# Kernel optimization log

Hardware: AMD Instinct MI355X
Metric: run time of the kernel (lower is better)

The kernel has to match this reference:

```python
import jax, jax.numpy as jnp
import numpy as np

B, S, D = 16, 2048, 512
CODEBOOK = 8192


def setup_inputs() -> dict:
    key = jax.random.key(0)
    k1, k2, k3 = jax.random.split(key, 3)
    x = jax.random.normal(k1, (B, S, D), dtype=jnp.float32)
    input_length = jax.random.randint(k2, (B,), 1, S + 1).astype(jnp.int32)
    # kaiming-uniform-ish init of the codebook
    bound = float(np.sqrt(6.0 / D))
    embed = jax.random.uniform(k3, (CODEBOOK, D), dtype=jnp.float32,
                               minval=-bound, maxval=bound)
    return {"x": x, "input_length": input_length, "embed": embed}


def reference(x, input_length, embed):
    # x: [B, S, D] float32, input_length: [B] int32, embed: [C, D] float32
    b, s, d = x.shape
    mask = jnp.arange(s)[None, :] < input_length[:, None]  # [B, S]
    x = x.astype(jnp.float32)

    # Euclidean cdist (clamped, sqrt), negated; argmax = nearest code.
    x2 = jnp.sum(x * x, axis=-1, keepdims=True)            # [B, S, 1]
    e2 = jnp.sum(embed * embed, axis=-1)                   # [C]
    xy = jnp.einsum('bsd,cd->bsc', x, embed)               # [B, S, C]
    dist = -jnp.sqrt(jnp.clip(x2 + e2[None, None, :] - 2.0 * xy, 0.0))

    embed_ind = jnp.argmax(dist, axis=-1)                  # [B, S] int
    quantize = embed[embed_ind]                            # [B, S, D]

    # pack/unpack in the torch code reduces to masking per-token results
    quantize = jnp.where(mask[..., None], quantize, 0.0)
    embed_ind = jnp.where(mask, embed_ind, -1)
    return quantize, embed_ind
```

## Files before the change

### kernel.cpp

```cpp
#include <hip/hip_runtime.h>
#include <cfloat>

typedef _Float16 half8  __attribute__((ext_vector_type(8)));
typedef short    bf16x8 __attribute__((ext_vector_type(8)));
typedef float    floatx4 __attribute__((ext_vector_type(4)));
typedef int      intx4  __attribute__((ext_vector_type(4)));
typedef unsigned long long ull;

#define NBATCH 16
#define NSEQ   2048
#define ND     512
#define NC     8192
#define NTOK   (NBATCH * NSEQ)
#define NTT    (NTOK / 128)
#define NCT    (NC / 128)
#define KQ     (ND / 64)
#define SEGY   8
#define MARGIN 0.35f

#define XSCALE 8.0f
#define ESCALE 64.0f
#define SCORE_SCALE (2.0f / (XSCALE * ESCALE))

typedef const void __attribute__((address_space(1)))* gp_t;
typedef void       __attribute__((address_space(3)))* lp_t;
__device__ __forceinline__ void cp16(lp_t l, gp_t g) {
  __builtin_amdgcn_global_load_lds(g, l, 16, 0, 0);
}

__global__ __launch_bounds__(256) void prep_embed(const float* __restrict__ embed,
                                                  char* __restrict__ qe,
                                                  float* __restrict__ se,
                                                  _Float16* __restrict__ eh,
                                                  _Float16* __restrict__ el,
                                                  float* __restrict__ e2) {
  int wave = threadIdx.x >> 6, lane = threadIdx.x & 63;
  int c = blockIdx.x * 4 + wave;
  const float* row = embed + (size_t)c * ND;
  float4 v0 = ((const float4*)row)[lane * 2];
  float4 v1 = ((const float4*)row)[lane * 2 + 1];
  float vs[8] = {v0.x, v0.y, v0.z, v0.w, v1.x, v1.y, v1.z, v1.w};
  float am = 0.f, s = 0.f;
#pragma unroll
  for (int q = 0; q < 8; ++q) { am = fmaxf(am, fabsf(vs[q])); s = fmaf(vs[q], vs[q], s); }
#pragma unroll
  for (int m = 1; m < 64; m <<= 1) {
    am = fmaxf(am, __shfl_xor(am, m, 64));
    s += __shfl_xor(s, m, 64);
  }
  float inv = am > 0.f ? 127.f / am : 0.f;
  ull pk = 0; half8 h, l;
#pragma unroll
  for (int q = 0; q < 8; ++q) {
    int qv = (int)rintf(vs[q] * inv);
    qv = min(127, max(-127, qv));
    pk |= (ull)(unsigned char)(signed char)qv << (8 * q);
    float sv = ESCALE * vs[q];
    _Float16 hh = (_Float16)sv;
    h[q] = hh;
    l[q] = (_Float16)(sv - (float)hh);
  }
  ((ull*)(qe + (size_t)c * ND))[lane] = pk;
  ((half8*)(eh + (size_t)c * ND))[lane] = h;
  ((half8*)(el + (size_t)c * ND))[lane] = l;
  if (lane == 0) { se[c] = am / 127.f; e2[c] = s; }
}

__global__ __launch_bounds__(256) void prep_xq(const float* __restrict__ x,
                                               char* __restrict__ qx,
                                               float* __restrict__ sx) {
  int wave = threadIdx.x >> 6, lane = threadIdx.x & 63;
  int t = blockIdx.x * 4 + wave;
  const float* row = x + (size_t)t * ND;
  float4 v0 = ((const float4*)row)[lane * 2];
  float4 v1 = ((const float4*)row)[lane * 2 + 1];
  float vs[8] = {v0.x, v0.y, v0.z, v0.w, v1.x, v1.y, v1.z, v1.w};
  float am = 0.f;
#pragma unroll
  for (int q = 0; q < 8; ++q) am = fmaxf(am, fabsf(vs[q]));
#pragma unroll
  for (int m = 1; m < 64; m <<= 1) am = fmaxf(am, __shfl_xor(am, m, 64));
  float inv = am > 0.f ? 127.f / am : 0.f;
  ull pk = 0;
#pragma unroll
  for (int q = 0; q < 8; ++q) {
    int qv = (int)rintf(vs[q] * inv);
    qv = min(127, max(-127, qv));
    pk |= (ull)(unsigned char)(signed char)qv << (8 * q);
  }
  ((ull*)(qx + (size_t)t * ND))[lane] = pk;
  if (lane == 0) sx[t] = am / 127.f;
}

__global__ __launch_bounds__(256) void vq_init(unsigned long long* __restrict__ pKey,
                                               int* __restrict__ cnt) {
  int i = blockIdx.x * 256 + threadIdx.x;
  pKey[i] = ~0ULL;
  if (i < NCT) cnt[i] = 0;
}

__global__ __launch_bounds__(256) void vq_approx(
    const char* __restrict__ qx, const float* __restrict__ sx,
    const int* __restrict__ len,
    const char* __restrict__ qe, const float* __restrict__ se,
    const float* __restrict__ e2g,
    float* __restrict__ tMin) {
  __shared__ char sXb[3][128 * 64];
  __shared__ char sEb[3][128 * 64];

  const int gid = blockIdx.x;
  const int tt = (gid >> 9) * 8 + (gid & 7);
  const int ct = (gid & 511) >> 3;
  const int b = tt >> 4, s0 = (tt & 15) * 128;
  if (s0 >= len[b]) return;
  const int row0 = tt * 128, code0 = ct * 128;

  const int tid = threadIdx.x, wave = tid >> 6, lane = tid & 63;
  const int quad = lane >> 4, lid = lane & 15;
  const int wr = wave >> 1, wc = wave & 1;

  const int r0 = tid >> 2;
  const int csrc = (tid & 3) ^ ((tid >> 3) & 3);
  const int ldsb0 = wave * 1024;
  const int ldsb1 = 4096 + wave * 1024;

  const int cswz = quad ^ ((lid >> 1) & 3);
  int aoff[4], boff[4];
#pragma unroll
  for (int i = 0; i < 4; ++i) aoff[i] = (wr * 64 + i * 16 + lid) * 64 + cswz * 16;
#pragma unroll
  for (int j = 0; j < 4; ++j) boff[j] = (wc * 64 + j * 16 + lid) * 64 + cswz * 16;

  const char* pxb = qx + (size_t)(row0 + r0) * ND + csrc * 16;
  const char* peb = qe + (size_t)(code0 + r0) * ND + csrc * 16;

  intx4 acc[4][4];
#pragma unroll
  for (int i = 0; i < 4; ++i)
#pragma unroll
    for (int j = 0; j < 4; ++j) acc[i][j] = (intx4){0, 0, 0, 0};

#define STAGE(bufi, kt) do { \
    cp16((lp_t)&sXb[bufi][ldsb0], (gp_t)(pxb + (kt) * 64)); \
    cp16((lp_t)&sXb[bufi][ldsb1], (gp_t)(pxb + 64 * ND + (kt) * 64)); \
    cp16((lp_t)&sEb[bufi][ldsb0], (gp_t)(peb + (kt) * 64)); \
    cp16((lp_t)&sEb[bufi][ldsb1], (gp_t)(peb + 64 * ND + (kt) * 64)); } while (0)

  STAGE(0, 0);
  STAGE(1, 1);
  asm volatile("s_waitcnt vmcnt(4)" ::: "memory");
  __builtin_amdgcn_s_barrier();

#pragma unroll
  for (int kt = 0; kt < KQ; ++kt) {
    const int buf = kt % 3;
    if (kt + 2 < KQ) STAGE((kt + 2) % 3, kt + 2);
    const char* A = sXb[buf];
    const char* B = sEb[buf];
    intx4 av[4], bv[4];
#pragma unroll
    for (int j = 0; j < 4; ++j) bv[j] = *(const intx4*)&B[boff[j]];
#pragma unroll
    for (int i = 0; i < 4; ++i) av[i] = *(const intx4*)&A[aoff[i]];
    __builtin_amdgcn_s_setprio(1);
#pragma unroll
    for (int i = 0; i < 4; ++i)
#pragma unroll
      for (int j = 0; j < 4; ++j)
        acc[i][j] = __builtin_amdgcn_mfma_i32_16x16x64_i8(av[i], bv[j], acc[i][j], 0, 0, 0);
    __builtin_amdgcn_s_setprio(0);
    if (kt < KQ - 1) {
      if (kt <= KQ - 3) { asm volatile("s_waitcnt vmcnt(4)" ::: "memory"); }
      else              { asm volatile("s_waitcnt vmcnt(0)" ::: "memory"); }
      __builtin_amdgcn_s_barrier();
    }
  }
#undef STAGE

  float e2v[4], sev[4];
#pragma unroll
  for (int j = 0; j < 4; ++j) {
    int col = code0 + wc * 64 + j * 16 + lid;
    e2v[j] = e2g[col];
    sev[j] = se[col];
  }

  __syncthreads();
  float* sc = (float*)&sXb[0][0];
#pragma unroll
  for (int i = 0; i < 4; ++i) {
#pragma unroll
    for (int reg = 0; reg < 4; ++reg) {
      int row = wr * 64 + i * 16 + quad * 4 + reg;
      float rs = 2.0f * sx[row0 + row];
      float best = fmaf(-rs * sev[0], (float)acc[i][0][reg], e2v[0]);
#pragma unroll
      for (int j = 1; j < 4; ++j)
        best = fminf(best, fmaf(-rs * sev[j], (float)acc[i][j][reg], e2v[j]));
#pragma unroll
      for (int m = 1; m < 16; m <<= 1) best = fminf(best, __shfl_xor(best, m, 64));
      if (lid == 0) sc[row * 2 + wc] = best;
    }
  }
  __syncthreads();
  if (tid < 128)
    tMin[(size_t)(row0 + tid) * NCT + ct] = fminf(sc[tid * 2], sc[tid * 2 + 1]);
}

__global__ __launch_bounds__(256) void vq_select(
    const int* __restrict__ len, const float* __restrict__ tMin,
    int* __restrict__ list, int* __restrict__ cnt) {
  int wave = threadIdx.x >> 6, lane = threadIdx.x & 63;
  int t = blockIdx.x * 4 + wave;
  int b = t >> 11, s = t & (NSEQ - 1);
  if (s >= len[b]) return;
  float v = tMin[(size_t)t * NCT + lane];
  float m = v;
#pragma unroll
  for (int d = 1; d < 64; d <<= 1) m = fminf(m, __shfl_xor(m, d, 64));
  if (v <= m + MARGIN) {
    int pos = atomicAdd(&cnt[lane], 1);
    list[lane * NTOK + pos] = t;
  }
}

__global__ __launch_bounds__(256, 1) void vq_rescore(
    const float* __restrict__ x,
    const _Float16* __restrict__ eh, const _Float16* __restrict__ el,
    const float* __restrict__ e2g,
    const int* __restrict__ list, const int* __restrict__ cnt,
    unsigned long long* __restrict__ pKey) {
  const int j = blockIdx.x;
  const int n = cnt[j];
  const int code0 = j * 128;

  const int tid = threadIdx.x, wave = tid >> 6, lane = tid & 63;
  const int quad = lane >> 4, lid = lane & 15;
  const int wr = wave >> 1, wc = wave & 1;

  float e2v[4]; int cjv[4];
#pragma unroll
  for (int jj = 0; jj < 4; ++jj) {
    cjv[jj] = code0 + wc * 64 + jj * 16 + lid;
    e2v[jj] = e2g[cjv[jj]];
  }

  for (int seg = blockIdx.y; seg * 128 < n; seg += SEGY) {
    const int base = seg * 128;
    int tok[4];
#pragma unroll
    for (int i = 0; i < 4; ++i)
      tok[i] = list[j * NTOK + min(base + wr * 64 + i * 16 + lid, n - 1)];

    floatx4 acc[4][4];
#pragma unroll
    for (int i = 0; i < 4; ++i)
#pragma unroll
      for (int jj = 0; jj < 4; ++jj) acc[i][jj] = (floatx4){0.f, 0.f, 0.f, 0.f};

    for (int kt = 0; kt < 16; kt += 2) {
      float4 af[2][4][2];
#pragma unroll
      for (int s = 0; s < 2; ++s)
#pragma unroll
        for (int i = 0; i < 4; ++i) {
          const float* px = x + (size_t)tok[i] * ND + (kt + s) * 32 + quad * 8;
          af[s][i][0] = *(const float4*)px;
          af[s][i][1] = *(const float4*)(px + 4);
        }
      half8 bh[2][4], bl[2][4];
#pragma unroll
      for (int s = 0; s < 2; ++s)
#pragma unroll
        for (int jj = 0; jj < 4; ++jj) {
          const size_t eo = (size_t)cjv[jj] * ND + (kt + s) * 32 + quad * 8;
          bh[s][jj] = *(const half8*)(eh + eo);
          bl[s][jj] = *(const half8*)(el + eo);
        }
#pragma unroll
      for (int s = 0; s < 2; ++s) {
        half8 ah[4], al[4];
#pragma unroll
        for (int i = 0; i < 4; ++i) {
          float vs[8] = {af[s][i][0].x, af[s][i][0].y, af[s][i][0].z, af[s][i][0].w,
                         af[s][i][1].x, af[s][i][1].y, af[s][i][1].z, af[s][i][1].w};
#pragma unroll
          for (int q = 0; q < 8; ++q) {
            float vv = XSCALE * vs[q];
            _Float16 hh = (_Float16)vv;
            ah[i][q] = hh;
            al[i][q] = (_Float16)(vv - (float)hh);
          }
        }
#pragma unroll
        for (int i = 0; i < 4; ++i)
#pragma unroll
          for (int jj = 0; jj < 4; ++jj) {
            acc[i][jj] = __builtin_amdgcn_mfma_f32_16x16x32_f16(ah[i], bh[s][jj], acc[i][jj], 0, 0, 0);
            acc[i][jj] = __builtin_amdgcn_mfma_f32_16x16x32_f16(ah[i], bl[s][jj], acc[i][jj], 0, 0, 0);
            acc[i][jj] = __builtin_amdgcn_mfma_f32_16x16x32_f16(al[i], bh[s][jj], acc[i][jj], 0, 0, 0);
          }
      }
    }

#pragma unroll
    for (int i = 0; i < 4; ++i) {
#pragma unroll
      for (int reg = 0; reg < 4; ++reg) {
        float best = fmaf(-SCORE_SCALE, acc[i][0][reg], e2v[0]);
        int bidx = cjv[0];
#pragma unroll
        for (int jj = 1; jj < 4; ++jj) {
          float vj = fmaf(-SCORE_SCALE, acc[i][jj][reg], e2v[jj]);
          if (vj < best) { best = vj; bidx = cjv[jj]; }
        }
#pragma unroll
        for (int m = 1; m < 16; m <<= 1) {
          float ov = __shfl_xor(best, m, 64);
          int   oi = __shfl_xor(bidx, m, 64);
          if (ov < best || (ov == best && oi < bidx)) { best = ov; bidx = oi; }
        }
        if (lid == 0) {
          int row = wr * 64 + i * 16 + quad * 4 + reg;
          int t = list[j * NTOK + min(base + row, n - 1)];
          if (best == 0.0f) best = 0.0f;
          unsigned u = __float_as_uint(best);
          u ^= (u >> 31) ? 0xFFFFFFFFu : 0x80000000u;
          unsigned long long key = ((unsigned long long)u << 32) | (unsigned)bidx;
          atomicMin(&pKey[t], key);
        }
      }
    }
  }
}

__global__ __launch_bounds__(256) void vq_output(
    const float* __restrict__ embed, const int* __restrict__ len,
    const unsigned long long* __restrict__ pKey,
    float* __restrict__ out) {
  int wave = threadIdx.x >> 6, lane = threadIdx.x & 63;
  int t = blockIdx.x * 4 + wave;
  int b = t >> 11, s = t & (NSEQ - 1);
  float* outq = out + (size_t)t * ND;
  float* outind = out + (size_t)NTOK * ND;
  if (s >= len[b]) {
    float4 z = {0.f, 0.f, 0.f, 0.f};
    *(float4*)&outq[lane * 8]     = z;
    *(float4*)&outq[lane * 8 + 4] = z;
    if (lane == 0) outind[t] = -1.0f;
    return;
  }
  unsigned long long key = pKey[t];
  int bi = (int)(unsigned)(key & 0xFFFFFFFFULL);
  const float* er = embed + (size_t)bi * ND;
  *(float4*)&outq[lane * 8]     = *(const float4*)&er[lane * 8];
  *(float4*)&outq[lane * 8 + 4] = *(const float4*)&er[lane * 8 + 4];
  if (lane == 0) outind[t] = (float)bi;
}

extern "C" void kernel_launch(void* const* d_in, const int* in_sizes, int n_in,
                              void* d_out, int out_size, void* d_ws, size_t ws_size,
                              hipStream_t stream) {
  const float* x     = (const float*)d_in[0];
  const int*   lenp  = (const int*)d_in[1];
  const float* embed = (const float*)d_in[2];
  float* out = (float*)d_out;

  char* w = (char*)d_ws;
  size_t off = 0;
  char*     qe = (char*)(w + off);     off += (size_t)NC * ND;
  float*    se = (float*)(w + off);    off += (size_t)NC * 4;
  _Float16* eh = (_Float16*)(w + off); off += (size_t)NC * ND * 2;
  _Float16* el = (_Float16*)(w + off); off += (size_t)NC * ND * 2;
  float*    e2 = (float*)(w + off);    off += (size_t)NC * 4;
  char*     qx = (char*)(w + off);     off += (size_t)NTOK * ND;
  float*    sx = (float*)(w + off);    off += (size_t)NTOK * 4;
  float*  tMin = (float*)(w + off);    off += (size_t)NTOK * NCT * 4;
  int*    list = (int*)(w + off);      off += (size_t)NCT * NTOK * 4;
  int*     cnt = (int*)(w + off);      off += 256;
  unsigned long long* pKey = (unsigned long long*)(w + off); off += (size_t)NTOK * 8;

  prep_embed<<<NC / 4, 256, 0, stream>>>(embed, qe, se, eh, el, e2);
  prep_xq<<<NTOK / 4, 256, 0, stream>>>(x, qx, sx);
  vq_init<<<NTOK / 256, 256, 0, stream>>>(pKey, cnt);
  vq_approx<<<NTT * NCT, 256, 0, stream>>>(qx, sx, lenp, qe, se, e2, tMin);
  vq_select<<<NTOK / 4, 256, 0, stream>>>(lenp, tMin, list, cnt);
  vq_rescore<<<dim3(NCT, SEGY), 256, 0, stream>>>(x, eh, el, e2, list, cnt, pKey);
  vq_output<<<NTOK / 4, 256, 0, stream>>>(embed, lenp, pKey, out);
}
```

Before: 457.8 us.

## Keep token int8 tile in registers and stream codebook chunks per block

Restructures the int8 approximate-distance GEMM. Each block now loads its 128-token A tile once into registers and loops over 16 codebook chunks of 128 codes, double-buffering full-K chunks of the codebook in LDS, instead of launching one block per 128x128 tile with a K-pipelined triple buffer. Blocks grow to 512 threads and the per-code norms and scales are staged in LDS. This removes repeated A-tile loads and per-tile launch overhead. In exchange it raises register pressure and LDS use (about 140KB per block, so likely one block per CU despite the launch bound of 2), and adds a barrier per chunk.

```diff
diff --git a/kernel.cpp b/kernel.cpp
--- a/kernel.cpp
+++ b/kernel.cpp
@@ -14,7 +14,6 @@
 #define NTOK   (NBATCH * NSEQ)
 #define NTT    (NTOK / 128)
 #define NCT    (NC / 128)
-#define KQ     (ND / 64)
 #define SEGY   8
 #define MARGIN 0.35f
 
@@ -99,112 +98,114 @@
   if (i < NCT) cnt[i] = 0;
 }
 
-__global__ __launch_bounds__(256) void vq_approx(
+__global__ __launch_bounds__(512, 2) void vq_approx(
     const char* __restrict__ qx, const float* __restrict__ sx,
     const int* __restrict__ len,
     const char* __restrict__ qe, const float* __restrict__ se,
     const float* __restrict__ e2g,
     float* __restrict__ tMin) {
-  __shared__ char sXb[3][128 * 64];
-  __shared__ char sEb[3][128 * 64];
-
-  const int gid = blockIdx.x;
-  const int tt = (gid >> 9) * 8 + (gid & 7);
-  const int ct = (gid & 511) >> 3;
+  __shared__ char  sB[2][65536];
+  __shared__ float sE2[2048];
+  __shared__ float sSe[2048];
+  __shared__ float sMin[128][4];
+
+  const int tt = blockIdx.x;
   const int b = tt >> 4, s0 = (tt & 15) * 128;
   if (s0 >= len[b]) return;
-  const int row0 = tt * 128, code0 = ct * 128;
-
-  const int tid = threadIdx.x, wave = tid >> 6, lane = tid & 63;
+  const int row0 = tt * 128;
+  const int code0 = blockIdx.y * 2048;
+
+  const int tid = threadIdx.x;
+  const int wave = tid >> 6, lane = tid & 63;
   const int quad = lane >> 4, lid = lane & 15;
-  const int wr = wave >> 1, wc = wave & 1;
-
-  const int r0 = tid >> 2;
-  const int csrc = (tid & 3) ^ ((tid >> 3) & 3);
-  const int ldsb0 = wave * 1024;
-  const int ldsb1 = 4096 + wave * 1024;
-
-  const int cswz = quad ^ ((lid >> 1) & 3);
-  int aoff[4], boff[4];
-#pragma unroll
-  for (int i = 0; i < 4; ++i) aoff[i] = (wr * 64 + i * 16 + lid) * 64 + cswz * 16;
-#pragma unroll
-  for (int j = 0; j < 4; ++j) boff[j] = (wc * 64 + j * 16 + lid) * 64 + cswz * 16;
-
-  const char* pxb = qx + (size_t)(row0 + r0) * ND + csrc * 16;
-  const char* peb = qe + (size_t)(code0 + r0) * ND + csrc * 16;
-
-  intx4 acc[4][4];
-#pragma unroll
-  for (int i = 0; i < 4; ++i)
-#pragma unroll
-    for (int j = 0; j < 4; ++j) acc[i][j] = (intx4){0, 0, 0, 0};
-
-#define STAGE(bufi, kt) do { \
-    cp16((lp_t)&sXb[bufi][ldsb0], (gp_t)(pxb + (kt) * 64)); \
-    cp16((lp_t)&sXb[bufi][ldsb1], (gp_t)(pxb + 64 * ND + (kt) * 64)); \
-    cp16((lp_t)&sEb[bufi][ldsb0], (gp_t)(peb + (kt) * 64)); \
-    cp16((lp_t)&sEb[bufi][ldsb1], (gp_t)(peb + 64 * ND + (kt) * 64)); } while (0)
-
+  const int wm = wave >> 2, wn = wave & 3;
+
+  const char* pa = qx + (size_t)(row0 + wm * 64 + lid) * ND + quad * 16;
+  intx4 a[4][8];
+#pragma unroll
+  for (int rt = 0; rt < 4; ++rt)
+#pragma unroll
+    for (int ks = 0; ks < 8; ++ks)
+      a[rt][ks] = *(const intx4*)(pa + rt * 16 * ND + ks * 64);
+
+  float4 sx4[4];
+#pragma unroll
+  for (int rt = 0; rt < 4; ++rt)
+    sx4[rt] = *(const float4*)&sx[row0 + wm * 64 + rt * 16 + quad * 4];
+
+  const char* pbs = qe + (size_t)(code0 + (tid >> 5)) * ND +
+                    (((tid & 31) ^ ((tid >> 5) & 7)) * 16);
+  const int ldsw = wave * 1024;
+
+#define STAGE(c, buf) do { \
+    _Pragma("unroll") \
+    for (int it = 0; it < 8; ++it) \
+      cp16((lp_t)&sB[buf][it * 8192 + ldsw], (gp_t)(pbs + ((c) * 128 + it * 16) * ND)); \
+  } while (0)
+
+  cp16((lp_t)((char*)sE2 + ldsw), (gp_t)((const char*)(e2g + code0) + tid * 16));
+  cp16((lp_t)((char*)sSe + ldsw), (gp_t)((const char*)(se + code0) + tid * 16));
   STAGE(0, 0);
   STAGE(1, 1);
-  asm volatile("s_waitcnt vmcnt(4)" ::: "memory");
+  asm volatile("s_waitcnt vmcnt(8)" ::: "memory");
   __builtin_amdgcn_s_barrier();
 
-#pragma unroll
-  for (int kt = 0; kt < KQ; ++kt) {
-    const int buf = kt % 3;
-    if (kt + 2 < KQ) STAGE((kt + 2) % 3, kt + 2);
-    const char* A = sXb[buf];
-    const char* B = sEb[buf];
-    intx4 av[4], bv[4];
-#pragma unroll
-    for (int j = 0; j < 4; ++j) bv[j] = *(const intx4*)&B[boff[j]];
-#pragma unroll
-    for (int i = 0; i < 4; ++i) av[i] = *(const intx4*)&A[aoff[i]];
+  const int xg = lid & 7;
+  const int rb0 = (wn * 32 + lid) * 512, rb1 = rb0 + 16 * 512;
+
+#pragma unroll 2
+  for (int c = 0; c < 16; ++c) {
+    const char* B = sB[c & 1];
+    intx4 acc[4][2];
+#pragma unroll
+    for (int rt = 0; rt < 4; ++rt) { acc[rt][0] = (intx4){0,0,0,0}; acc[rt][1] = (intx4){0,0,0,0}; }
+
     __builtin_amdgcn_s_setprio(1);
 #pragma unroll
-    for (int i = 0; i < 4; ++i)
-#pragma unroll
-      for (int j = 0; j < 4; ++j)
-        acc[i][j] = __builtin_amdgcn_mfma_i32_16x16x64_i8(av[i], bv[j], acc[i][j], 0, 0, 0);
+    for (int ks = 0; ks < 8; ++ks) {
+      const int p = (((ks * 4 + quad) ^ xg) * 16);
+      intx4 b0 = *(const intx4*)&B[rb0 + p];
+      intx4 b1 = *(const intx4*)&B[rb1 + p];
+#pragma unroll
+      for (int rt = 0; rt < 4; ++rt) {
+        acc[rt][0] = __builtin_amdgcn_mfma_i32_16x16x64_i8(a[rt][ks], b0, acc[rt][0], 0, 0, 0);
+        acc[rt][1] = __builtin_amdgcn_mfma_i32_16x16x64_i8(a[rt][ks], b1, acc[rt][1], 0, 0, 0);
+      }
+    }
     __builtin_amdgcn_s_setprio(0);
-    if (kt < KQ - 1) {
-      if (kt <= KQ - 3) { asm volatile("s_waitcnt vmcnt(4)" ::: "memory"); }
-      else              { asm volatile("s_waitcnt vmcnt(0)" ::: "memory"); }
-      __builtin_amdgcn_s_barrier();
-    }
+
+    const int cl = c * 128 + wn * 32 + lid;
+    const float e2v0 = sE2[cl], e2v1 = sE2[cl + 16];
+    const float sv0 = sSe[cl], sv1 = sSe[cl + 16];
+#pragma unroll
+    for (int rt = 0; rt < 4; ++rt) {
+#pragma unroll
+      for (int reg = 0; reg < 4; ++reg) {
+        const float rs = 2.0f * sx4[rt][reg];
+        float best = fminf(fmaf(-rs * sv0, (float)acc[rt][0][reg], e2v0),
+                           fmaf(-rs * sv1, (float)acc[rt][1][reg], e2v1));
+#pragma unroll
+        for (int m = 1; m < 16; m <<= 1) best = fminf(best, __shfl_xor(best, m, 64));
+        if (lid == 0) sMin[wm * 64 + rt * 16 + quad * 4 + reg][wn] = best;
+      }
+    }
+    asm volatile("s_waitcnt lgkmcnt(0)" ::: "memory");
+    __builtin_amdgcn_s_barrier();
+
+    if (tid < 128) {
+      float4 v = *(const float4*)sMin[tid];
+      float mn = fminf(fminf(v.x, v.y), fminf(v.z, v.w));
+      tMin[(size_t)(row0 + tid) * NCT + (blockIdx.y * 16 + c)] = mn;
+    }
+    if (c + 2 < 16) {
+      STAGE(c + 2, c & 1);
+      asm volatile("s_waitcnt vmcnt(8)" ::: "memory");
+    } else if (c + 1 < 16) {
+      asm volatile("s_waitcnt vmcnt(0)" ::: "memory");
+    }
+    if (c + 1 < 16) __builtin_amdgcn_s_barrier();
   }
 #undef STAGE
-
-  float e2v[4], sev[4];
-#pragma unroll
-  for (int j = 0; j < 4; ++j) {
-    int col = code0 + wc * 64 + j * 16 + lid;
-    e2v[j] = e2g[col];
-    sev[j] = se[col];
-  }
-
-  __syncthreads();
-  float* sc = (float*)&sXb[0][0];
-#pragma unroll
-  for (int i = 0; i < 4; ++i) {
-#pragma unroll
-    for (int reg = 0; reg < 4; ++reg) {
-      int row = wr * 64 + i * 16 + quad * 4 + reg;
-      float rs = 2.0f * sx[row0 + row];
-      float best = fmaf(-rs * sev[0], (float)acc[i][0][reg], e2v[0]);
-#pragma unroll
-      for (int j = 1; j < 4; ++j)
-        best = fminf(best, fmaf(-rs * sev[j], (float)acc[i][j][reg], e2v[j]));
-#pragma unroll
-      for (int m = 1; m < 16; m <<= 1) best = fminf(best, __shfl_xor(best, m, 64));
-      if (lid == 0) sc[row * 2 + wc] = best;
-    }
-  }
-  __syncthreads();
-  if (tid < 128)
-    tMin[(size_t)(row0 + tid) * NCT + ct] = fminf(sc[tid * 2], sc[tid * 2 + 1]);
 }
 
 __global__ __launch_bounds__(256) void vq_select(
@@ -383,7 +384,7 @@
   prep_embed<<<NC / 4, 256, 0, stream>>>(embed, qe, se, eh, el, e2);
   prep_xq<<<NTOK / 4, 256, 0, stream>>>(x, qx, sx);
   vq_init<<<NTOK / 256, 256, 0, stream>>>(pKey, cnt);
-  vq_approx<<<NTT * NCT, 256, 0, stream>>>(qx, sx, lenp, qe, se, e2, tMin);
+  vq_approx<<<dim3(NTT, 4), 512, 0, stream>>>(qx, sx, lenp, qe, se, e2, tMin);
   vq_select<<<NTOK / 4, 256, 0, stream>>>(lenp, tMin, list, cnt);
   vq_rescore<<<dim3(NCT, SEGY), 256, 0, stream>>>(x, eh, el, e2, list, cnt, pKey);
   vq_output<<<NTOK / 4, 256, 0, stream>>>(embed, lenp, pKey, out);
```

Result: slower. 619.0 us (+35.2%).

## Deepen int8 GEMM pipeline to four stages and simplify epilogue row-min reduction

Applied to the files above, without the earlier changes.

Raises the approximate int8 scoring kernel's LDS pipeline from three to four buffers, prefetching three K-tiles ahead and adjusting vmcnt waits to match. The epilogue now loads per-row scales as float4 and writes all per-lane partial minima to padded shared memory, so one thread per row reduces them instead of using cross-lane shuffles. The rescore kernel gets more segment blocks in y and exits early when a block has no work. Together these aim to hide more global-load latency and cut epilogue shuffle cost, at the price of 16KB more LDS per block, which may lower occupancy.

```diff
diff --git a/kernel.cpp b/kernel.cpp
--- a/kernel.cpp
+++ b/kernel.cpp
@@ -2,7 +2,6 @@
 #include <cfloat>
 
 typedef _Float16 half8  __attribute__((ext_vector_type(8)));
-typedef short    bf16x8 __attribute__((ext_vector_type(8)));
 typedef float    floatx4 __attribute__((ext_vector_type(4)));
 typedef int      intx4  __attribute__((ext_vector_type(4)));
 typedef unsigned long long ull;
@@ -15,7 +14,7 @@
 #define NTT    (NTOK / 128)
 #define NCT    (NC / 128)
 #define KQ     (ND / 64)
-#define SEGY   8
+#define SEGY   16
 #define MARGIN 0.35f
 
 #define XSCALE 8.0f
@@ -105,8 +104,8 @@
     const char* __restrict__ qe, const float* __restrict__ se,
     const float* __restrict__ e2g,
     float* __restrict__ tMin) {
-  __shared__ char sXb[3][128 * 64];
-  __shared__ char sEb[3][128 * 64];
+  __shared__ char sXb[4][128 * 64];
+  __shared__ char sEb[4][128 * 64];
 
   const int gid = blockIdx.x;
   const int tt = (gid >> 9) * 8 + (gid & 7);
@@ -148,13 +147,14 @@
 
   STAGE(0, 0);
   STAGE(1, 1);
-  asm volatile("s_waitcnt vmcnt(4)" ::: "memory");
+  STAGE(2, 2);
+  asm volatile("s_waitcnt vmcnt(8)" ::: "memory");
   __builtin_amdgcn_s_barrier();
 
 #pragma unroll
   for (int kt = 0; kt < KQ; ++kt) {
-    const int buf = kt % 3;
-    if (kt + 2 < KQ) STAGE((kt + 2) % 3, kt + 2);
+    const int buf = kt & 3;
+    if (kt + 3 < KQ) STAGE((kt + 3) & 3, kt + 3);
     const char* A = sXb[buf];
     const char* B = sEb[buf];
     intx4 av[4], bv[4];
@@ -170,8 +170,9 @@
         acc[i][j] = __builtin_amdgcn_mfma_i32_16x16x64_i8(av[i], bv[j], acc[i][j], 0, 0, 0);
     __builtin_amdgcn_s_setprio(0);
     if (kt < KQ - 1) {
-      if (kt <= KQ - 3) { asm volatile("s_waitcnt vmcnt(4)" ::: "memory"); }
-      else              { asm volatile("s_waitcnt vmcnt(0)" ::: "memory"); }
+      if (kt + 3 < KQ)      { asm volatile("s_waitcnt vmcnt(8)" ::: "memory"); }
+      else if (kt + 2 < KQ) { asm volatile("s_waitcnt vmcnt(4)" ::: "memory"); }
+      else                  { asm volatile("s_waitcnt vmcnt(0)" ::: "memory"); }
       __builtin_amdgcn_s_barrier();
     }
   }
@@ -184,27 +185,34 @@
     e2v[j] = e2g[col];
     sev[j] = se[col];
   }
+  float4 sx4[4];
+#pragma unroll
+  for (int i = 0; i < 4; ++i)
+    sx4[i] = *(const float4*)&sx[row0 + wr * 64 + i * 16 + quad * 4];
 
   __syncthreads();
-  float* sc = (float*)&sXb[0][0];
+  float* pm = (float*)&sXb[0][0];
 #pragma unroll
   for (int i = 0; i < 4; ++i) {
 #pragma unroll
     for (int reg = 0; reg < 4; ++reg) {
-      int row = wr * 64 + i * 16 + quad * 4 + reg;
-      float rs = 2.0f * sx[row0 + row];
+      const int row = wr * 64 + i * 16 + quad * 4 + reg;
+      const float rs = 2.0f * sx4[i][reg];
       float best = fmaf(-rs * sev[0], (float)acc[i][0][reg], e2v[0]);
 #pragma unroll
       for (int j = 1; j < 4; ++j)
         best = fminf(best, fmaf(-rs * sev[j], (float)acc[i][j][reg], e2v[j]));
-#pragma unroll
-      for (int m = 1; m < 16; m <<= 1) best = fminf(best, __shfl_xor(best, m, 64));
-      if (lid == 0) sc[row * 2 + wc] = best;
+      pm[row * 33 + wc * 16 + lid] = best;
     }
   }
   __syncthreads();
-  if (tid < 128)
-    tMin[(size_t)(row0 + tid) * NCT + ct] = fminf(sc[tid * 2], sc[tid * 2 + 1]);
+  if (tid < 128) {
+    const float* r = pm + tid * 33;
+    float mn = r[0];
+#pragma unroll
+    for (int k = 1; k < 32; ++k) mn = fminf(mn, r[k]);
+    tMin[(size_t)(row0 + tid) * NCT + ct] = mn;
+  }
 }
 
 __global__ __launch_bounds__(256) void vq_select(
@@ -233,6 +241,7 @@
   const int j = blockIdx.x;
   const int n = cnt[j];
   const int code0 = j * 128;
+  if ((int)blockIdx.y * 128 >= n) return;
 
   const int tid = threadIdx.x, wave = tid >> 6, lane = tid & 63;
   const int quad = lane >> 4, lid = lane & 15;
```

Result: faster. 428.5 us (-6.4%).
